# Performance work log

Measured on AMD Instinct MI355X. Metric: run time of the kernel, lower is better.

Reference implementation:

```python
import jax, jax.numpy as jnp
import numpy as np

B, T, D, H = 64, 512, 1024, 1024
FORGET_BIAS = 1.0  # tf BasicLSTMCell default


def setup_inputs() -> dict:
    key = jax.random.key(0)
    k1, k2 = jax.random.split(key)
    x = jax.random.normal(k1, (B, T, D), dtype=jnp.float32)
    W = jax.random.normal(k2, (D + H, 4 * H), dtype=jnp.float32) * 0.01  # W_stddev
    b = jnp.full((4 * H,), 0.1, dtype=jnp.float32)  # b_val
    return {"x": x, "W": W, "b": b}


def reference(x, W, b):
    # Unrolled BasicLSTMCell over num_of_cells steps, expressed as lax.scan.
    # Gate order (i, j, f, o), new_c = c*sigmoid(f+1) + sigmoid(i)*tanh(j),
    # new_h = tanh(new_c)*sigmoid(o). return_cell_out=True -> [B, T, H].
    Bx = x.shape[0]
    h0 = jnp.zeros((Bx, H), dtype=x.dtype)
    c0 = jnp.zeros((Bx, H), dtype=x.dtype)

    def step(carry, xt):  # xt: [B, D]
        c, h = carry
        z = jnp.concatenate([xt, h], axis=-1) @ W + b  # [B, 4H]
        i, j, f, o = jnp.split(z, 4, axis=-1)
        c_new = c * jax.nn.sigmoid(f + FORGET_BIAS) + jax.nn.sigmoid(i) * jnp.tanh(j)
        h_new = jnp.tanh(c_new) * jax.nn.sigmoid(o)
        return (c_new, h_new), h_new

    xs = jnp.swapaxes(x, 0, 1)  # [T, B, D]
    (_, _), hs = jax.lax.scan(step, (c0, h0), xs)  # hs: [T, B, H]
    return jnp.swapaxes(hs, 0, 1)  # [B, T, H]
```

## Files before the change

kernel.cpp:

```cpp
#include <hip/hip_runtime.h>
#include <hip/hip_bf16.h>

#define BB 64
#define TT 512
#define DD 1024
#define HH 1024

typedef __bf16 bf16x8 __attribute__((ext_vector_type(8)));
typedef float floatx4 __attribute__((ext_vector_type(4)));

__device__ __forceinline__ float sigmoidf_fast(float x) {
    return 1.0f / (1.0f + __expf(-x));
}
__device__ __forceinline__ float tanhf_fast(float x) {
    return 1.0f - 2.0f / (__expf(2.0f * x) + 1.0f);
}

__device__ __forceinline__ bool detect_f32(const void* bias) {
    return *(const unsigned*)bias == 0x3DCCCCCDu;
}

__global__ __launch_bounds__(256) void cvt_x_kernel(const void* __restrict__ xin,
                                                    const void* __restrict__ bias,
                                                    __bf16* __restrict__ xc) {
    const bool f32 = detect_f32(bias);
    size_t i = ((size_t)blockIdx.x * 256 + threadIdx.x) * 8;
    bf16x8 r;
    if (f32) {
        const float* p = (const float*)xin + i;
        float4 a = *(const float4*)p;
        float4 b = *(const float4*)(p + 4);
        r[0] = (__bf16)a.x; r[1] = (__bf16)a.y; r[2] = (__bf16)a.z; r[3] = (__bf16)a.w;
        r[4] = (__bf16)b.x; r[5] = (__bf16)b.y; r[6] = (__bf16)b.z; r[7] = (__bf16)b.w;
    } else {
        r = *(const bf16x8*)((const __bf16*)xin + i);
    }
    *(bf16x8*)(xc + i) = r;
}

#define HLOAD16(P, O0, O1, O2, O3, O4, O5, O6, O7, O8, O9, O10, O11, O12, O13, O14, O15, \
                h0, h1, h2, h3, h4, h5, h6, h7, h8, h9, h10, h11, h12, h13, h14, h15)     \
    asm volatile(                                                                         \
        "global_load_dwordx4 %0, %16, off offset:" #O0 " sc0 sc1\n\t"                     \
        "global_load_dwordx4 %1, %16, off offset:" #O1 " sc0 sc1\n\t"                     \
        "global_load_dwordx4 %2, %16, off offset:" #O2 " sc0 sc1\n\t"                     \
        "global_load_dwordx4 %3, %16, off offset:" #O3 " sc0 sc1\n\t"                     \
        "global_load_dwordx4 %4, %16, off offset:" #O4 " sc0 sc1\n\t"                     \
        "global_load_dwordx4 %5, %16, off offset:" #O5 " sc0 sc1\n\t"                     \
        "global_load_dwordx4 %6, %16, off offset:" #O6 " sc0 sc1\n\t"                     \
        "global_load_dwordx4 %7, %16, off offset:" #O7 " sc0 sc1\n\t"                     \
        "global_load_dwordx4 %8, %16, off offset:" #O8 " sc0 sc1\n\t"                     \
        "global_load_dwordx4 %9, %16, off offset:" #O9 " sc0 sc1\n\t"                     \
        "global_load_dwordx4 %10, %16, off offset:" #O10 " sc0 sc1\n\t"                   \
        "global_load_dwordx4 %11, %16, off offset:" #O11 " sc0 sc1\n\t"                   \
        "global_load_dwordx4 %12, %16, off offset:" #O12 " sc0 sc1\n\t"                   \
        "global_load_dwordx4 %13, %16, off offset:" #O13 " sc0 sc1\n\t"                   \
        "global_load_dwordx4 %14, %16, off offset:" #O14 " sc0 sc1\n\t"                   \
        "global_load_dwordx4 %15, %16, off offset:" #O15 " sc0 sc1"                       \
        : "=v"(h0), "=v"(h1), "=v"(h2), "=v"(h3), "=v"(h4), "=v"(h5), "=v"(h6), "=v"(h7), \
          "=v"(h8), "=v"(h9), "=v"(h10), "=v"(h11), "=v"(h12), "=v"(h13), "=v"(h14),      \
          "=v"(h15)                                                                       \
        : "v"(P)                                                                          \
        : "memory");                                                                      \
    asm volatile("s_waitcnt vmcnt(0)"                                                     \
        : "+v"(h0), "+v"(h1), "+v"(h2), "+v"(h3), "+v"(h4), "+v"(h5), "+v"(h6), "+v"(h7), \
          "+v"(h8), "+v"(h9), "+v"(h10), "+v"(h11), "+v"(h12), "+v"(h13), "+v"(h14),      \
          "+v"(h15));

#define HMFMA(HV, KC)                                                                 \
    acc = __builtin_amdgcn_mfma_f32_16x16x32_bf16(                                    \
        __builtin_bit_cast(bf16x8, HV),                                               \
        *(const bf16x8*)&Wlds[(((KC) + 32) * 64 + lane) * 8], acc, 0, 0, 0);

template <bool XCONV>
__global__ __launch_bounds__(256, 1)
void lstm_persistent(const void* __restrict__ x_raw,
                     const void* __restrict__ W_raw,
                     const void* __restrict__ bias_raw,
                     void* __restrict__ out_raw,
                     unsigned int* __restrict__ cnt,
                     __bf16* __restrict__ hbuf,
                     const __bf16* __restrict__ xc)
{
    const int tid  = threadIdx.x;
    const int bk   = blockIdx.x;
    const int wave = tid >> 6;
    const int lane = tid & 63;
    const int quad = lane >> 4;
    const int c    = lane & 15;
    const bool f32 = detect_f32(bias_raw);

    __shared__ __bf16 Wlds[64 * 64 * 8];
    for (int it = 0; it < 32; ++it) {
        int idx = it * 256 + tid;
        int k = idx >> 2, g = idx & 3;
        __bf16 w0, w1, w2, w3;
        if (f32) {
            float4 w4 = *(const float4*)((const float*)W_raw + k * 4096 + g * 1024 + bk * 4);
            w0 = (__bf16)w4.x; w1 = (__bf16)w4.y; w2 = (__bf16)w4.z; w3 = (__bf16)w4.w;
        } else {
            const __bf16* wp = (const __bf16*)W_raw + k * 4096 + g * 1024 + bk * 4;
            w0 = wp[0]; w1 = wp[1]; w2 = wp[2]; w3 = wp[3];
        }
        int kc = k >> 5, q = (k >> 3) & 3, j = k & 7;
        int base = (kc * 64 + q * 16 + g * 4) * 8 + j;
        Wlds[base]      = w0;
        Wlds[base + 8]  = w1;
        Wlds[base + 16] = w2;
        Wlds[base + 24] = w3;
    }
    __syncthreads();

    const int rowA  = wave * 16 + c;
    const int nOut  = bk * 4 + (c & 3);
    const int orow  = wave * 16 + (lane >> 2);
    const int ocol  = bk * 4 + (lane & 3);

    float bi, bj, bfg, bo;
    if (f32) {
        const float* bp = (const float*)bias_raw;
        bi = bp[nOut]; bj = bp[1024 + nOut]; bfg = bp[2048 + nOut] + 1.0f; bo = bp[3072 + nOut];
    } else {
        const __bf16* bp = (const __bf16*)bias_raw;
        bi = (float)bp[nOut]; bj = (float)bp[1024 + nOut];
        bfg = (float)bp[2048 + nOut] + 1.0f; bo = (float)bp[3072 + nOut];
    }

    float cst[4] = {0.f, 0.f, 0.f, 0.f};

    const __bf16* xcA = xc + (size_t)rowA * (TT * DD) + quad * 8;
    const float*  xfA = (const float*)x_raw + (size_t)rowA * (TT * DD) + quad * 8;
    float* outf = (float*)out_raw;
    __hip_bfloat16* outb = (__hip_bfloat16*)out_raw;

    for (int t = 0; t < TT; ++t) {
        floatx4 acc = {0.f, 0.f, 0.f, 0.f};

#pragma unroll 8
        for (int kc = 0; kc < 32; ++kc) {
            bf16x8 a;
            if (XCONV) {
                a = *(const bf16x8*)(xcA + (size_t)t * DD + kc * 32);
            } else {
                const float* p = xfA + (size_t)t * DD + kc * 32;
                float4 u = *(const float4*)p;
                float4 v = *(const float4*)(p + 4);
                a[0] = (__bf16)u.x; a[1] = (__bf16)u.y; a[2] = (__bf16)u.z; a[3] = (__bf16)u.w;
                a[4] = (__bf16)v.x; a[5] = (__bf16)v.y; a[6] = (__bf16)v.z; a[7] = (__bf16)v.w;
            }
            bf16x8 w = *(const bf16x8*)&Wlds[(kc * 64 + lane) * 8];
            acc = __builtin_amdgcn_mfma_f32_16x16x32_bf16(a, w, acc, 0, 0, 0);
        }

        if (t > 0) {
            if (tid == 0) {
                while (__hip_atomic_load(&cnt[t - 1], __ATOMIC_RELAXED,
                                         __HIP_MEMORY_SCOPE_AGENT) < 256u)
                    __builtin_amdgcn_s_sleep(2);
            }
            __syncthreads();
            const __bf16* hp = hbuf + (size_t)(t & 1) * (BB * HH)
                             + (size_t)rowA * HH + quad * 8;
            floatx4 h0, h1, h2, h3, h4, h5, h6, h7, h8, h9, h10, h11, h12, h13, h14, h15;
            HLOAD16(hp, 0, 64, 128, 192, 256, 320, 384, 448, 512, 576, 640, 704, 768,
                    832, 896, 960,
                    h0, h1, h2, h3, h4, h5, h6, h7, h8, h9, h10, h11, h12, h13, h14, h15)
            HMFMA(h0, 0)  HMFMA(h1, 1)  HMFMA(h2, 2)   HMFMA(h3, 3)
            HMFMA(h4, 4)  HMFMA(h5, 5)  HMFMA(h6, 6)   HMFMA(h7, 7)
            HMFMA(h8, 8)  HMFMA(h9, 9)  HMFMA(h10, 10) HMFMA(h11, 11)
            HMFMA(h12, 12) HMFMA(h13, 13) HMFMA(h14, 14) HMFMA(h15, 15)
            HLOAD16(hp, 1024, 1088, 1152, 1216, 1280, 1344, 1408, 1472, 1536, 1600,
                    1664, 1728, 1792, 1856, 1920, 1984,
                    h0, h1, h2, h3, h4, h5, h6, h7, h8, h9, h10, h11, h12, h13, h14, h15)
            HMFMA(h0, 16)  HMFMA(h1, 17)  HMFMA(h2, 18)  HMFMA(h3, 19)
            HMFMA(h4, 20)  HMFMA(h5, 21)  HMFMA(h6, 22)  HMFMA(h7, 23)
            HMFMA(h8, 24)  HMFMA(h9, 25)  HMFMA(h10, 26) HMFMA(h11, 27)
            HMFMA(h12, 28) HMFMA(h13, 29) HMFMA(h14, 30) HMFMA(h15, 31)
        }

        float hv0, hv1, hv2, hv3;
        {
#pragma unroll
            for (int r = 0; r < 4; ++r) {
                float av = acc[r];
                float jg = __shfl(av, (lane + 4) & 63, 64);
                float fg = __shfl(av, (lane + 8) & 63, 64);
                float og = __shfl(av, (lane + 12) & 63, 64);
                float I = sigmoidf_fast(av + bi);
                float J = tanhf_fast(jg + bj);
                float F = sigmoidf_fast(fg + bfg);
                float O = sigmoidf_fast(og + bo);
                float cc = cst[r] * F + I * J;
                cst[r] = cc;
                float hvr = tanhf_fast(cc) * O;
                if (r == 0) hv0 = hvr; else if (r == 1) hv1 = hvr;
                else if (r == 2) hv2 = hvr; else hv3 = hvr;
            }
        }

        int srcLane = (lane & 48) | (lane & 3);
        float t0 = __shfl(hv0, srcLane, 64);
        float t1 = __shfl(hv1, srcLane, 64);
        float t2 = __shfl(hv2, srcLane, 64);
        float t3 = __shfl(hv3, srcLane, 64);
        int rsel = (lane >> 2) & 3;
        float va = (rsel & 1) ? t1 : t0;
        float vb = (rsel & 1) ? t3 : t2;
        float hvf = (rsel & 2) ? vb : va;

        size_t oidx = (size_t)orow * (TT * HH) + (size_t)t * HH + ocol;
        if (f32) outf[oidx] = hvf;
        else     outb[oidx] = __float2bfloat16(hvf);

        {
            __bf16 hb = (__bf16)hvf;
            unsigned hbits = (unsigned)__builtin_bit_cast(unsigned short, hb);
            const __bf16* hwp = hbuf + (size_t)((t + 1) & 1) * (BB * HH)
                              + (size_t)orow * HH + ocol;
            asm volatile("global_store_short %0, %1, off sc0 sc1"
                         :: "v"(hwp), "v"(hbits) : "memory");
        }

        asm volatile("s_waitcnt vmcnt(0)" ::: "memory");
        __syncthreads();
        if (tid == 0) atomicAdd(&cnt[t], 1u);
    }
}

extern "C" void kernel_launch(void* const* d_in, const int* in_sizes, int n_in,
                              void* d_out, int out_size, void* d_ws, size_t ws_size,
                              hipStream_t stream) {
    const void* x = d_in[0];
    const void* W = d_in[1];
    const void* b = d_in[2];

    unsigned int* cnt = (unsigned int*)d_ws;
    __bf16*      hbuf = (__bf16*)((char*)d_ws + 4096);
    __bf16*      xc   = (__bf16*)((char*)d_ws + 266240);

    const size_t need = 266240 + (size_t)BB * TT * DD * 2;

    hipMemsetAsync(d_ws, 0, TT * sizeof(unsigned int), stream);
    if (ws_size >= need) {
        cvt_x_kernel<<<(BB * TT * DD / 8 + 255) / 256, 256, 0, stream>>>(x, b, xc);
        lstm_persistent<true><<<256, 256, 0, stream>>>(x, W, b, d_out, cnt, hbuf, xc);
    } else {
        lstm_persistent<false><<<256, 256, 0, stream>>>(x, W, b, d_out, cnt, hbuf, xc);
    }
}
```

Measured before the change: 5.651 ms.

## Split waves into x-projection and recurrent roles with per-wave flag sync

Halves the grid to 128 blocks of 512 threads, each owning 8 hidden columns. Four waves compute the input projection for step t while the other four wait on the previous step's h and run the recurrent MFMAs; partial sums are exchanged through LDS. The single atomic counter and block-wide barrier are replaced by per-wave flag words that are polled with vector loads. The h loads are also split into two batches with partial waits so MFMAs can start sooner. This aims to take the x-projection off the recurrent critical path and cut barrier latency, at the cost of a larger flag area that must be zeroed by memset and a block-wide barrier at every step.

Result: slower. 6.625 ms (+17.2%).

```diff
diff --git a/kernel.cpp b/kernel.cpp
--- a/kernel.cpp
+++ b/kernel.cpp
@@ -5,9 +5,12 @@
 #define TT 512
 #define DD 1024
 #define HH 1024
+#define NB 128
+#define NTHR 512
 
 typedef __bf16 bf16x8 __attribute__((ext_vector_type(8)));
 typedef float floatx4 __attribute__((ext_vector_type(4)));
+typedef unsigned int uintx4 __attribute__((ext_vector_type(4)));
 
 __device__ __forceinline__ float sigmoidf_fast(float x) {
     return 1.0f / (1.0f + __expf(-x));
@@ -38,8 +41,8 @@
     *(bf16x8*)(xc + i) = r;
 }
 
-#define HLOAD16(P, O0, O1, O2, O3, O4, O5, O6, O7, O8, O9, O10, O11, O12, O13, O14, O15, \
-                h0, h1, h2, h3, h4, h5, h6, h7, h8, h9, h10, h11, h12, h13, h14, h15)     \
+#define HISSUE16(P, O0, O1, O2, O3, O4, O5, O6, O7, O8, O9, O10, O11, O12, O13, O14, O15, \
+                 h0, h1, h2, h3, h4, h5, h6, h7, h8, h9, h10, h11, h12, h13, h14, h15)    \
     asm volatile(                                                                         \
         "global_load_dwordx4 %0, %16, off offset:" #O0 " sc0 sc1\n\t"                     \
         "global_load_dwordx4 %1, %16, off offset:" #O1 " sc0 sc1\n\t"                     \
@@ -57,53 +60,115 @@
         "global_load_dwordx4 %13, %16, off offset:" #O13 " sc0 sc1\n\t"                   \
         "global_load_dwordx4 %14, %16, off offset:" #O14 " sc0 sc1\n\t"                   \
         "global_load_dwordx4 %15, %16, off offset:" #O15 " sc0 sc1"                       \
-        : "=v"(h0), "=v"(h1), "=v"(h2), "=v"(h3), "=v"(h4), "=v"(h5), "=v"(h6), "=v"(h7), \
-          "=v"(h8), "=v"(h9), "=v"(h10), "=v"(h11), "=v"(h12), "=v"(h13), "=v"(h14),      \
-          "=v"(h15)                                                                       \
+        : "=&v"(h0), "=&v"(h1), "=&v"(h2), "=&v"(h3), "=&v"(h4), "=&v"(h5), "=&v"(h6),    \
+          "=&v"(h7), "=&v"(h8), "=&v"(h9), "=&v"(h10), "=&v"(h11), "=&v"(h12),            \
+          "=&v"(h13), "=&v"(h14), "=&v"(h15)                                              \
         : "v"(P)                                                                          \
-        : "memory");                                                                      \
-    asm volatile("s_waitcnt vmcnt(0)"                                                     \
+        : "memory");
+
+#define HWAIT16(N, h0, h1, h2, h3, h4, h5, h6, h7, h8, h9, h10, h11, h12, h13, h14, h15)  \
+    asm volatile("s_waitcnt vmcnt(" #N ")"                                                \
         : "+v"(h0), "+v"(h1), "+v"(h2), "+v"(h3), "+v"(h4), "+v"(h5), "+v"(h6), "+v"(h7), \
           "+v"(h8), "+v"(h9), "+v"(h10), "+v"(h11), "+v"(h12), "+v"(h13), "+v"(h14),      \
           "+v"(h15));
 
-#define HMFMA(HV, KC)                                                                 \
-    acc = __builtin_amdgcn_mfma_f32_16x16x32_bf16(                                    \
-        __builtin_bit_cast(bf16x8, HV),                                               \
-        *(const bf16x8*)&Wlds[(((KC) + 32) * 64 + lane) * 8], acc, 0, 0, 0);
+#define HMFMA2(HV, KCG)                                                            \
+    acc0 = __builtin_amdgcn_mfma_f32_16x16x32_bf16(                                \
+        __builtin_bit_cast(bf16x8, HV),                                            \
+        *(const bf16x8*)&Wlds[(((KCG) * 2 + 0) * 64 + lane) * 8], acc0, 0, 0, 0);  \
+    acc1 = __builtin_amdgcn_mfma_f32_16x16x32_bf16(                                \
+        __builtin_bit_cast(bf16x8, HV),                                            \
+        *(const bf16x8*)&Wlds[(((KCG) * 2 + 1) * 64 + lane) * 8], acc1, 0, 0, 0);
+
+#define GATES(ACC, BI, BJ, BFg, BO, C0, C1, C2, C3, HVF)                           \
+    {                                                                              \
+        float hv0, hv1, hv2, hv3;                                                  \
+        { float av = ACC[0];                                                       \
+          float jg = __shfl(av, (lane + 4) & 63, 64);                              \
+          float fg = __shfl(av, (lane + 8) & 63, 64);                              \
+          float og = __shfl(av, (lane + 12) & 63, 64);                             \
+          float I = sigmoidf_fast(av + BI);                                        \
+          float J = tanhf_fast(jg + BJ);                                           \
+          float F = sigmoidf_fast(fg + BFg);                                       \
+          float O = sigmoidf_fast(og + BO);                                        \
+          float cc = C0 * F + I * J; C0 = cc; hv0 = tanhf_fast(cc) * O; }          \
+        { float av = ACC[1];                                                       \
+          float jg = __shfl(av, (lane + 4) & 63, 64);                              \
+          float fg = __shfl(av, (lane + 8) & 63, 64);                              \
+          float og = __shfl(av, (lane + 12) & 63, 64);                             \
+          float I = sigmoidf_fast(av + BI);                                        \
+          float J = tanhf_fast(jg + BJ);                                           \
+          float F = sigmoidf_fast(fg + BFg);                                       \
+          float O = sigmoidf_fast(og + BO);                                        \
+          float cc = C1 * F + I * J; C1 = cc; hv1 = tanhf_fast(cc) * O; }          \
+        { float av = ACC[2];                                                       \
+          float jg = __shfl(av, (lane + 4) & 63, 64);                              \
+          float fg = __shfl(av, (lane + 8) & 63, 64);                              \
+          float og = __shfl(av, (lane + 12) & 63, 64);                             \
+          float I = sigmoidf_fast(av + BI);                                        \
+          float J = tanhf_fast(jg + BJ);                                           \
+          float F = sigmoidf_fast(fg + BFg);                                       \
+          float O = sigmoidf_fast(og + BO);                                        \
+          float cc = C2 * F + I * J; C2 = cc; hv2 = tanhf_fast(cc) * O; }          \
+        { float av = ACC[3];                                                       \
+          float jg = __shfl(av, (lane + 4) & 63, 64);                              \
+          float fg = __shfl(av, (lane + 8) & 63, 64);                              \
+          float og = __shfl(av, (lane + 12) & 63, 64);                             \
+          float I = sigmoidf_fast(av + BI);                                        \
+          float J = tanhf_fast(jg + BJ);                                           \
+          float F = sigmoidf_fast(fg + BFg);                                       \
+          float O = sigmoidf_fast(og + BO);                                        \
+          float cc = C3 * F + I * J; C3 = cc; hv3 = tanhf_fast(cc) * O; }          \
+        int srcLane = (lane & 48) | (lane & 3);                                    \
+        float t0 = __shfl(hv0, srcLane, 64);                                       \
+        float t1 = __shfl(hv1, srcLane, 64);                                       \
+        float t2 = __shfl(hv2, srcLane, 64);                                       \
+        float t3 = __shfl(hv3, srcLane, 64);                                       \
+        int rsel = (lane >> 2) & 3;                                                \
+        float va = (rsel & 1) ? t1 : t0;                                           \
+        float vb = (rsel & 1) ? t3 : t2;                                           \
+        HVF = (rsel & 2) ? vb : va;                                                \
+    }
 
 template <bool XCONV>
-__global__ __launch_bounds__(256, 1)
+__global__ __launch_bounds__(NTHR, 1)
 void lstm_persistent(const void* __restrict__ x_raw,
                      const void* __restrict__ W_raw,
                      const void* __restrict__ bias_raw,
                      void* __restrict__ out_raw,
-                     unsigned int* __restrict__ cnt,
+                     unsigned int* __restrict__ flags,
                      __bf16* __restrict__ hbuf,
                      const __bf16* __restrict__ xc)
 {
-    const int tid  = threadIdx.x;
-    const int bk   = blockIdx.x;
-    const int wave = tid >> 6;
-    const int lane = tid & 63;
-    const int quad = lane >> 4;
-    const int c    = lane & 15;
-    const bool f32 = detect_f32(bias_raw);
-
-    __shared__ __bf16 Wlds[64 * 64 * 8];
+    const int tid   = threadIdx.x;
+    const int bk    = blockIdx.x;
+    const int wave  = tid >> 6;
+    const int lane  = tid & 63;
+    const int quad  = lane >> 4;
+    const int c     = lane & 15;
+    const bool f32  = detect_f32(bias_raw);
+    const bool hrole = wave < 4;
+    const int wr    = wave & 3;
+
+    __shared__ __bf16 Wlds[64 * 2 * 512];
+    __shared__ float  xpart[2][4][2][64][4];
+
     for (int it = 0; it < 32; ++it) {
-        int idx = it * 256 + tid;
-        int k = idx >> 2, g = idx & 3;
+        int idx = it * NTHR + tid;
+        int n   = idx >> 13;
+        int r   = idx & 8191;
+        int k   = r >> 2, g = r & 3;
+        int col = g * 1024 + bk * 8 + n * 4;
         __bf16 w0, w1, w2, w3;
         if (f32) {
-            float4 w4 = *(const float4*)((const float*)W_raw + k * 4096 + g * 1024 + bk * 4);
+            float4 w4 = *(const float4*)((const float*)W_raw + (size_t)k * 4096 + col);
             w0 = (__bf16)w4.x; w1 = (__bf16)w4.y; w2 = (__bf16)w4.z; w3 = (__bf16)w4.w;
         } else {
-            const __bf16* wp = (const __bf16*)W_raw + k * 4096 + g * 1024 + bk * 4;
+            const __bf16* wp = (const __bf16*)W_raw + (size_t)k * 4096 + col;
             w0 = wp[0]; w1 = wp[1]; w2 = wp[2]; w3 = wp[3];
         }
         int kc = k >> 5, q = (k >> 3) & 3, j = k & 7;
-        int base = (kc * 64 + q * 16 + g * 4) * 8 + j;
+        int base = (((kc * 2 + n) * 64) + q * 16 + g * 4) * 8 + j;
         Wlds[base]      = w0;
         Wlds[base + 8]  = w1;
         Wlds[base + 16] = w2;
@@ -111,22 +176,29 @@
     }
     __syncthreads();
 
-    const int rowA  = wave * 16 + c;
-    const int nOut  = bk * 4 + (c & 3);
-    const int orow  = wave * 16 + (lane >> 2);
-    const int ocol  = bk * 4 + (lane & 3);
-
-    float bi, bj, bfg, bo;
-    if (f32) {
-        const float* bp = (const float*)bias_raw;
-        bi = bp[nOut]; bj = bp[1024 + nOut]; bfg = bp[2048 + nOut] + 1.0f; bo = bp[3072 + nOut];
-    } else {
-        const __bf16* bp = (const __bf16*)bias_raw;
-        bi = (float)bp[nOut]; bj = (float)bp[1024 + nOut];
-        bfg = (float)bp[2048 + nOut] + 1.0f; bo = (float)bp[3072 + nOut];
-    }
-
-    float cst[4] = {0.f, 0.f, 0.f, 0.f};
+    const int rowA = wr * 16 + c;
+    const int orow = wr * 16 + (lane >> 2);
+    const int oc0  = bk * 8 + (lane & 3);
+    const int oc1  = oc0 + 4;
+
+    float bi0, bj0, bf0, bo0, bi1, bj1, bf1, bo1;
+    float cA0 = 0.f, cA1 = 0.f, cA2 = 0.f, cA3 = 0.f;
+    float cB0 = 0.f, cB1 = 0.f, cB2 = 0.f, cB3 = 0.f;
+    if (hrole) {
+        int n0 = bk * 8 + (c & 3);
+        int n1 = n0 + 4;
+        if (f32) {
+            const float* bp = (const float*)bias_raw;
+            bi0 = bp[n0]; bj0 = bp[1024 + n0]; bf0 = bp[2048 + n0] + 1.0f; bo0 = bp[3072 + n0];
+            bi1 = bp[n1]; bj1 = bp[1024 + n1]; bf1 = bp[2048 + n1] + 1.0f; bo1 = bp[3072 + n1];
+        } else {
+            const __bf16* bp = (const __bf16*)bias_raw;
+            bi0 = (float)bp[n0]; bj0 = (float)bp[1024 + n0];
+            bf0 = (float)bp[2048 + n0] + 1.0f; bo0 = (float)bp[3072 + n0];
+            bi1 = (float)bp[n1]; bj1 = (float)bp[1024 + n1];
+            bf1 = (float)bp[2048 + n1] + 1.0f; bo1 = (float)bp[3072 + n1];
+        }
+    }
 
     const __bf16* xcA = xc + (size_t)rowA * (TT * DD) + quad * 8;
     const float*  xfA = (const float*)x_raw + (size_t)rowA * (TT * DD) + quad * 8;
@@ -134,96 +206,102 @@
     __hip_bfloat16* outb = (__hip_bfloat16*)out_raw;
 
     for (int t = 0; t < TT; ++t) {
-        floatx4 acc = {0.f, 0.f, 0.f, 0.f};
-
+        const int p = t & 1;
+        floatx4 acc0 = {0.f, 0.f, 0.f, 0.f};
+        floatx4 acc1 = {0.f, 0.f, 0.f, 0.f};
+
+        if (!hrole) {
+            floatx4 a0 = {0.f, 0.f, 0.f, 0.f};
+            floatx4 a1 = {0.f, 0.f, 0.f, 0.f};
 #pragma unroll 8
-        for (int kc = 0; kc < 32; ++kc) {
-            bf16x8 a;
-            if (XCONV) {
-                a = *(const bf16x8*)(xcA + (size_t)t * DD + kc * 32);
+            for (int kc = 0; kc < 32; ++kc) {
+                bf16x8 a;
+                if (XCONV) {
+                    a = *(const bf16x8*)(xcA + (size_t)t * DD + kc * 32);
+                } else {
+                    const float* pp = xfA + (size_t)t * DD + kc * 32;
+                    float4 u = *(const float4*)pp;
+                    float4 v = *(const float4*)(pp + 4);
+                    a[0] = (__bf16)u.x; a[1] = (__bf16)u.y; a[2] = (__bf16)u.z; a[3] = (__bf16)u.w;
+                    a[4] = (__bf16)v.x; a[5] = (__bf16)v.y; a[6] = (__bf16)v.z; a[7] = (__bf16)v.w;
+                }
+                a0 = __builtin_amdgcn_mfma_f32_16x16x32_bf16(
+                    a, *(const bf16x8*)&Wlds[((kc * 2 + 0) * 64 + lane) * 8], a0, 0, 0, 0);
+                a1 = __builtin_amdgcn_mfma_f32_16x16x32_bf16(
+                    a, *(const bf16x8*)&Wlds[((kc * 2 + 1) * 64 + lane) * 8], a1, 0, 0, 0);
+            }
+            *(floatx4*)&xpart[p][wr][0][lane][0] = a0;
+            *(floatx4*)&xpart[p][wr][1][lane][0] = a1;
+        } else if (t > 0) {
+            const unsigned int* fp = flags + (size_t)(t - 1) * 512 + (lane << 3);
+            for (;;) {
+                uintx4 fa, fb;
+                asm volatile(
+                    "global_load_dwordx4 %0, %2, off sc0 sc1\n\t"
+                    "global_load_dwordx4 %1, %2, off offset:16 sc0 sc1\n\t"
+                    "s_waitcnt vmcnt(0)"
+                    : "=&v"(fa), "=&v"(fb) : "v"(fp) : "memory");
+                unsigned ok = fa[0] & fa[1] & fa[2] & fa[3] & fb[0] & fb[1] & fb[2] & fb[3];
+                if (__all((int)ok)) break;
+                __builtin_amdgcn_s_sleep(1);
+            }
+            const __bf16* hp = hbuf + (size_t)(t & 1) * (BB * HH) + (size_t)rowA * HH + quad * 8;
+            floatx4 h0, h1, h2, h3, h4, h5, h6, h7, h8, h9, h10, h11, h12, h13, h14, h15;
+            floatx4 g0, g1, g2, g3, g4, g5, g6, g7, g8, g9, g10, g11, g12, g13, g14, g15;
+            HISSUE16(hp, 0, 64, 128, 192, 256, 320, 384, 448, 512, 576, 640, 704, 768,
+                     832, 896, 960,
+                     h0, h1, h2, h3, h4, h5, h6, h7, h8, h9, h10, h11, h12, h13, h14, h15)
+            HISSUE16(hp, 1024, 1088, 1152, 1216, 1280, 1344, 1408, 1472, 1536, 1600,
+                     1664, 1728, 1792, 1856, 1920, 1984,
+                     g0, g1, g2, g3, g4, g5, g6, g7, g8, g9, g10, g11, g12, g13, g14, g15)
+            HWAIT16(16, h0, h1, h2, h3, h4, h5, h6, h7, h8, h9, h10, h11, h12, h13, h14, h15)
+            HMFMA2(h0, 32)  HMFMA2(h1, 33)  HMFMA2(h2, 34)  HMFMA2(h3, 35)
+            HMFMA2(h4, 36)  HMFMA2(h5, 37)  HMFMA2(h6, 38)  HMFMA2(h7, 39)
+            HMFMA2(h8, 40)  HMFMA2(h9, 41)  HMFMA2(h10, 42) HMFMA2(h11, 43)
+            HMFMA2(h12, 44) HMFMA2(h13, 45) HMFMA2(h14, 46) HMFMA2(h15, 47)
+            HWAIT16(0, g0, g1, g2, g3, g4, g5, g6, g7, g8, g9, g10, g11, g12, g13, g14, g15)
+            HMFMA2(g0, 48)  HMFMA2(g1, 49)  HMFMA2(g2, 50)  HMFMA2(g3, 51)
+            HMFMA2(g4, 52)  HMFMA2(g5, 53)  HMFMA2(g6, 54)  HMFMA2(g7, 55)
+            HMFMA2(g8, 56)  HMFMA2(g9, 57)  HMFMA2(g10, 58) HMFMA2(g11, 59)
+            HMFMA2(g12, 60) HMFMA2(g13, 61) HMFMA2(g14, 62) HMFMA2(g15, 63)
+        }
+
+        __syncthreads();
+
+        if (hrole) {
+            acc0 += *(const floatx4*)&xpart[p][wr][0][lane][0];
+            acc1 += *(const floatx4*)&xpart[p][wr][1][lane][0];
+
+            float hvf0, hvf1;
+            GATES(acc0, bi0, bj0, bf0, bo0, cA0, cA1, cA2, cA3, hvf0)
+            GATES(acc1, bi1, bj1, bf1, bo1, cB0, cB1, cB2, cB3, hvf1)
+
+            {
+                __bf16 hb0 = (__bf16)hvf0, hb1 = (__bf16)hvf1;
+                unsigned b0 = (unsigned)__builtin_bit_cast(unsigned short, hb0);
+                unsigned b1 = (unsigned)__builtin_bit_cast(unsigned short, hb1);
+                const __bf16* hw = hbuf + (size_t)((t + 1) & 1) * (BB * HH) + (size_t)orow * HH;
+                asm volatile(
+                    "global_store_short %0, %2, off sc0 sc1\n\t"
+                    "global_store_short %1, %3, off sc0 sc1"
+                    :: "v"(hw + oc0), "v"(hw + oc1), "v"(b0), "v"(b1) : "memory");
+            }
+            asm volatile("s_waitcnt vmcnt(0)" ::: "memory");
+            if (lane == 0) {
+                unsigned one = 1u;
+                const unsigned int* fw = flags + (size_t)t * 512 + (bk * 4 + wr);
+                asm volatile("global_store_dword %0, %1, off sc0 sc1"
+                             :: "v"(fw), "v"(one) : "memory");
+            }
+            size_t ob = (size_t)orow * (TT * HH) + (size_t)t * HH;
+            if (f32) {
+                outf[ob + oc0] = hvf0;
+                outf[ob + oc1] = hvf1;
             } else {
-                const float* p = xfA + (size_t)t * DD + kc * 32;
-                float4 u = *(const float4*)p;
-                float4 v = *(const float4*)(p + 4);
-                a[0] = (__bf16)u.x; a[1] = (__bf16)u.y; a[2] = (__bf16)u.z; a[3] = (__bf16)u.w;
-                a[4] = (__bf16)v.x; a[5] = (__bf16)v.y; a[6] = (__bf16)v.z; a[7] = (__bf16)v.w;
-            }
-            bf16x8 w = *(const bf16x8*)&Wlds[(kc * 64 + lane) * 8];
-            acc = __builtin_amdgcn_mfma_f32_16x16x32_bf16(a, w, acc, 0, 0, 0);
+                outb[ob + oc0] = __float2bfloat16(hvf0);
+                outb[ob + oc1] = __float2bfloat16(hvf1);
+            }
         }
-
-        if (t > 0) {
-            if (tid == 0) {
-                while (__hip_atomic_load(&cnt[t - 1], __ATOMIC_RELAXED,
-                                         __HIP_MEMORY_SCOPE_AGENT) < 256u)
-                    __builtin_amdgcn_s_sleep(2);
-            }
-            __syncthreads();
-            const __bf16* hp = hbuf + (size_t)(t & 1) * (BB * HH)
-                             + (size_t)rowA * HH + quad * 8;
-            floatx4 h0, h1, h2, h3, h4, h5, h6, h7, h8, h9, h10, h11, h12, h13, h14, h15;
-            HLOAD16(hp, 0, 64, 128, 192, 256, 320, 384, 448, 512, 576, 640, 704, 768,
-                    832, 896, 960,
-                    h0, h1, h2, h3, h4, h5, h6, h7, h8, h9, h10, h11, h12, h13, h14, h15)
-            HMFMA(h0, 0)  HMFMA(h1, 1)  HMFMA(h2, 2)   HMFMA(h3, 3)
-            HMFMA(h4, 4)  HMFMA(h5, 5)  HMFMA(h6, 6)   HMFMA(h7, 7)
-            HMFMA(h8, 8)  HMFMA(h9, 9)  HMFMA(h10, 10) HMFMA(h11, 11)
-            HMFMA(h12, 12) HMFMA(h13, 13) HMFMA(h14, 14) HMFMA(h15, 15)
-            HLOAD16(hp, 1024, 1088, 1152, 1216, 1280, 1344, 1408, 1472, 1536, 1600,
-                    1664, 1728, 1792, 1856, 1920, 1984,
-                    h0, h1, h2, h3, h4, h5, h6, h7, h8, h9, h10, h11, h12, h13, h14, h15)
-            HMFMA(h0, 16)  HMFMA(h1, 17)  HMFMA(h2, 18)  HMFMA(h3, 19)
-            HMFMA(h4, 20)  HMFMA(h5, 21)  HMFMA(h6, 22)  HMFMA(h7, 23)
-            HMFMA(h8, 24)  HMFMA(h9, 25)  HMFMA(h10, 26) HMFMA(h11, 27)
-            HMFMA(h12, 28) HMFMA(h13, 29) HMFMA(h14, 30) HMFMA(h15, 31)
-        }
-
-        float hv0, hv1, hv2, hv3;
-        {
-#pragma unroll
-            for (int r = 0; r < 4; ++r) {
-                float av = acc[r];
-                float jg = __shfl(av, (lane + 4) & 63, 64);
-                float fg = __shfl(av, (lane + 8) & 63, 64);
-                float og = __shfl(av, (lane + 12) & 63, 64);
-                float I = sigmoidf_fast(av + bi);
-                float J = tanhf_fast(jg + bj);
-                float F = sigmoidf_fast(fg + bfg);
-                float O = sigmoidf_fast(og + bo);
-                float cc = cst[r] * F + I * J;
-                cst[r] = cc;
-                float hvr = tanhf_fast(cc) * O;
-                if (r == 0) hv0 = hvr; else if (r == 1) hv1 = hvr;
-                else if (r == 2) hv2 = hvr; else hv3 = hvr;
-            }
-        }
-
-        int srcLane = (lane & 48) | (lane & 3);
-        float t0 = __shfl(hv0, srcLane, 64);
-        float t1 = __shfl(hv1, srcLane, 64);
-        float t2 = __shfl(hv2, srcLane, 64);
-        float t3 = __shfl(hv3, srcLane, 64);
-        int rsel = (lane >> 2) & 3;
-        float va = (rsel & 1) ? t1 : t0;
-        float vb = (rsel & 1) ? t3 : t2;
-        float hvf = (rsel & 2) ? vb : va;
-
-        size_t oidx = (size_t)orow * (TT * HH) + (size_t)t * HH + ocol;
-        if (f32) outf[oidx] = hvf;
-        else     outb[oidx] = __float2bfloat16(hvf);
-
-        {
-            __bf16 hb = (__bf16)hvf;
-            unsigned hbits = (unsigned)__builtin_bit_cast(unsigned short, hb);
-            const __bf16* hwp = hbuf + (size_t)((t + 1) & 1) * (BB * HH)
-                              + (size_t)orow * HH + ocol;
-            asm volatile("global_store_short %0, %1, off sc0 sc1"
-                         :: "v"(hwp), "v"(hbits) : "memory");
-        }
-
-        asm volatile("s_waitcnt vmcnt(0)" ::: "memory");
-        __syncthreads();
-        if (tid == 0) atomicAdd(&cnt[t], 1u);
     }
 }
 
@@ -234,17 +312,17 @@
     const void* W = d_in[1];
     const void* b = d_in[2];
 
-    unsigned int* cnt = (unsigned int*)d_ws;
-    __bf16*      hbuf = (__bf16*)((char*)d_ws + 4096);
-    __bf16*      xc   = (__bf16*)((char*)d_ws + 266240);
-
-    const size_t need = 266240 + (size_t)BB * TT * DD * 2;
-
-    hipMemsetAsync(d_ws, 0, TT * sizeof(unsigned int), stream);
+    unsigned int* flags = (unsigned int*)d_ws;
+    __bf16*      hbuf   = (__bf16*)((char*)d_ws + 1048576);
+    __bf16*      xc     = (__bf16*)((char*)d_ws + 1310720);
+
+    const size_t need = 1310720 + (size_t)BB * TT * DD * 2;
+
+    hipMemsetAsync(d_ws, 0, 1048576, stream);
     if (ws_size >= need) {
         cvt_x_kernel<<<(BB * TT * DD / 8 + 255) / 256, 256, 0, stream>>>(x, b, xc);
-        lstm_persistent<true><<<256, 256, 0, stream>>>(x, W, b, d_out, cnt, hbuf, xc);
+        lstm_persistent<true><<<NB, NTHR, 0, stream>>>(x, W, b, d_out, flags, hbuf, xc);
     } else {
-        lstm_persistent<false><<<256, 256, 0, stream>>>(x, W, b, d_out, cnt, hbuf, xc);
-    }
-}
+        lstm_persistent<false><<<NB, NTHR, 0, stream>>>(x, W, b, d_out, flags, hbuf, xc);
+    }
+}
```

## Split grid barrier into padded group counters and pipeline h loads with dual accumulators

Applied to the files above, without the earlier changes.

The single per-step atomic counter becomes 16 group counters padded onto separate cache lines, one per 16 blocks. Wave 0 polls all 16 in parallel with a wave-wide vote, which cuts contention on a single hot address. All 32 h loads are issued up front with a partial vmcnt wait, so the second half's latency overlaps the first half's MFMAs. Accumulation is split across two accumulators to shorten the MFMA dependency chain. The cost is a larger workspace and memset, plus more live registers.

Result: slower. 5.813 ms (+2.9%).

```diff
diff --git a/kernel.cpp b/kernel.cpp
--- a/kernel.cpp
+++ b/kernel.cpp
@@ -5,6 +5,8 @@
 #define TT 512
 #define DD 1024
 #define HH 1024
+#define NG 16
+#define GSTRIDE 32
 
 typedef __bf16 bf16x8 __attribute__((ext_vector_type(8)));
 typedef float floatx4 __attribute__((ext_vector_type(4)));
@@ -38,8 +40,8 @@
     *(bf16x8*)(xc + i) = r;
 }
 
-#define HLOAD16(P, O0, O1, O2, O3, O4, O5, O6, O7, O8, O9, O10, O11, O12, O13, O14, O15, \
-                h0, h1, h2, h3, h4, h5, h6, h7, h8, h9, h10, h11, h12, h13, h14, h15)     \
+#define HISSUE16(P, O0, O1, O2, O3, O4, O5, O6, O7, O8, O9, O10, O11, O12, O13, O14, O15, \
+                 h0, h1, h2, h3, h4, h5, h6, h7, h8, h9, h10, h11, h12, h13, h14, h15)    \
     asm volatile(                                                                         \
         "global_load_dwordx4 %0, %16, off offset:" #O0 " sc0 sc1\n\t"                     \
         "global_load_dwordx4 %1, %16, off offset:" #O1 " sc0 sc1\n\t"                     \
@@ -57,20 +59,22 @@
         "global_load_dwordx4 %13, %16, off offset:" #O13 " sc0 sc1\n\t"                   \
         "global_load_dwordx4 %14, %16, off offset:" #O14 " sc0 sc1\n\t"                   \
         "global_load_dwordx4 %15, %16, off offset:" #O15 " sc0 sc1"                       \
-        : "=v"(h0), "=v"(h1), "=v"(h2), "=v"(h3), "=v"(h4), "=v"(h5), "=v"(h6), "=v"(h7), \
-          "=v"(h8), "=v"(h9), "=v"(h10), "=v"(h11), "=v"(h12), "=v"(h13), "=v"(h14),      \
-          "=v"(h15)                                                                       \
+        : "=&v"(h0), "=&v"(h1), "=&v"(h2), "=&v"(h3), "=&v"(h4), "=&v"(h5), "=&v"(h6),    \
+          "=&v"(h7), "=&v"(h8), "=&v"(h9), "=&v"(h10), "=&v"(h11), "=&v"(h12),            \
+          "=&v"(h13), "=&v"(h14), "=&v"(h15)                                              \
         : "v"(P)                                                                          \
-        : "memory");                                                                      \
-    asm volatile("s_waitcnt vmcnt(0)"                                                     \
+        : "memory");
+
+#define HWAIT16(N, h0, h1, h2, h3, h4, h5, h6, h7, h8, h9, h10, h11, h12, h13, h14, h15)  \
+    asm volatile("s_waitcnt vmcnt(" #N ")"                                                \
         : "+v"(h0), "+v"(h1), "+v"(h2), "+v"(h3), "+v"(h4), "+v"(h5), "+v"(h6), "+v"(h7), \
           "+v"(h8), "+v"(h9), "+v"(h10), "+v"(h11), "+v"(h12), "+v"(h13), "+v"(h14),      \
           "+v"(h15));
 
-#define HMFMA(HV, KC)                                                                 \
-    acc = __builtin_amdgcn_mfma_f32_16x16x32_bf16(                                    \
-        __builtin_bit_cast(bf16x8, HV),                                               \
-        *(const bf16x8*)&Wlds[(((KC) + 32) * 64 + lane) * 8], acc, 0, 0, 0);
+#define HMFMA(ACC, HV, KC)                                                          \
+    ACC = __builtin_amdgcn_mfma_f32_16x16x32_bf16(                                  \
+        __builtin_bit_cast(bf16x8, HV),                                             \
+        *(const bf16x8*)&Wlds[(((KC) + 32) * 64 + lane) * 8], ACC, 0, 0, 0);
 
 template <bool XCONV>
 __global__ __launch_bounds__(256, 1)
@@ -78,7 +82,7 @@
                      const void* __restrict__ W_raw,
                      const void* __restrict__ bias_raw,
                      void* __restrict__ out_raw,
-                     unsigned int* __restrict__ cnt,
+                     unsigned int* __restrict__ gcnt,
                      __bf16* __restrict__ hbuf,
                      const __bf16* __restrict__ xc)
 {
@@ -134,7 +138,8 @@
     __hip_bfloat16* outb = (__hip_bfloat16*)out_raw;
 
     for (int t = 0; t < TT; ++t) {
-        floatx4 acc = {0.f, 0.f, 0.f, 0.f};
+        floatx4 accA = {0.f, 0.f, 0.f, 0.f};
+        floatx4 accB = {0.f, 0.f, 0.f, 0.f};
 
 #pragma unroll 8
         for (int kc = 0; kc < 32; ++kc) {
@@ -149,34 +154,49 @@
                 a[4] = (__bf16)v.x; a[5] = (__bf16)v.y; a[6] = (__bf16)v.z; a[7] = (__bf16)v.w;
             }
             bf16x8 w = *(const bf16x8*)&Wlds[(kc * 64 + lane) * 8];
-            acc = __builtin_amdgcn_mfma_f32_16x16x32_bf16(a, w, acc, 0, 0, 0);
+            if (kc & 1)
+                accB = __builtin_amdgcn_mfma_f32_16x16x32_bf16(a, w, accB, 0, 0, 0);
+            else
+                accA = __builtin_amdgcn_mfma_f32_16x16x32_bf16(a, w, accA, 0, 0, 0);
         }
 
         if (t > 0) {
-            if (tid == 0) {
-                while (__hip_atomic_load(&cnt[t - 1], __ATOMIC_RELAXED,
-                                         __HIP_MEMORY_SCOPE_AGENT) < 256u)
-                    __builtin_amdgcn_s_sleep(2);
+            if (wave == 0) {
+                const unsigned int* gp =
+                    gcnt + (size_t)(t - 1) * (NG * GSTRIDE) + (size_t)(lane & 15) * GSTRIDE;
+                for (;;) {
+                    unsigned v = NG;
+                    if (lane < NG)
+                        v = __hip_atomic_load(gp, __ATOMIC_RELAXED, __HIP_MEMORY_SCOPE_AGENT);
+                    if (__all((int)(v >= NG))) break;
+                    __builtin_amdgcn_s_sleep(1);
+                }
             }
             __syncthreads();
+
             const __bf16* hp = hbuf + (size_t)(t & 1) * (BB * HH)
                              + (size_t)rowA * HH + quad * 8;
             floatx4 h0, h1, h2, h3, h4, h5, h6, h7, h8, h9, h10, h11, h12, h13, h14, h15;
-            HLOAD16(hp, 0, 64, 128, 192, 256, 320, 384, 448, 512, 576, 640, 704, 768,
-                    832, 896, 960,
-                    h0, h1, h2, h3, h4, h5, h6, h7, h8, h9, h10, h11, h12, h13, h14, h15)
-            HMFMA(h0, 0)  HMFMA(h1, 1)  HMFMA(h2, 2)   HMFMA(h3, 3)
-            HMFMA(h4, 4)  HMFMA(h5, 5)  HMFMA(h6, 6)   HMFMA(h7, 7)
-            HMFMA(h8, 8)  HMFMA(h9, 9)  HMFMA(h10, 10) HMFMA(h11, 11)
-            HMFMA(h12, 12) HMFMA(h13, 13) HMFMA(h14, 14) HMFMA(h15, 15)
-            HLOAD16(hp, 1024, 1088, 1152, 1216, 1280, 1344, 1408, 1472, 1536, 1600,
-                    1664, 1728, 1792, 1856, 1920, 1984,
-                    h0, h1, h2, h3, h4, h5, h6, h7, h8, h9, h10, h11, h12, h13, h14, h15)
-            HMFMA(h0, 16)  HMFMA(h1, 17)  HMFMA(h2, 18)  HMFMA(h3, 19)
-            HMFMA(h4, 20)  HMFMA(h5, 21)  HMFMA(h6, 22)  HMFMA(h7, 23)
-            HMFMA(h8, 24)  HMFMA(h9, 25)  HMFMA(h10, 26) HMFMA(h11, 27)
-            HMFMA(h12, 28) HMFMA(h13, 29) HMFMA(h14, 30) HMFMA(h15, 31)
-        }
+            floatx4 g0, g1, g2, g3, g4, g5, g6, g7, g8, g9, g10, g11, g12, g13, g14, g15;
+            HISSUE16(hp, 0, 64, 128, 192, 256, 320, 384, 448, 512, 576, 640, 704, 768,
+                     832, 896, 960,
+                     h0, h1, h2, h3, h4, h5, h6, h7, h8, h9, h10, h11, h12, h13, h14, h15)
+            HISSUE16(hp, 1024, 1088, 1152, 1216, 1280, 1344, 1408, 1472, 1536, 1600,
+                     1664, 1728, 1792, 1856, 1920, 1984,
+                     g0, g1, g2, g3, g4, g5, g6, g7, g8, g9, g10, g11, g12, g13, g14, g15)
+            HWAIT16(16, h0, h1, h2, h3, h4, h5, h6, h7, h8, h9, h10, h11, h12, h13, h14, h15)
+            HMFMA(accA, h0, 0)   HMFMA(accB, h1, 1)   HMFMA(accA, h2, 2)   HMFMA(accB, h3, 3)
+            HMFMA(accA, h4, 4)   HMFMA(accB, h5, 5)   HMFMA(accA, h6, 6)   HMFMA(accB, h7, 7)
+            HMFMA(accA, h8, 8)   HMFMA(accB, h9, 9)   HMFMA(accA, h10, 10) HMFMA(accB, h11, 11)
+            HMFMA(accA, h12, 12) HMFMA(accB, h13, 13) HMFMA(accA, h14, 14) HMFMA(accB, h15, 15)
+            HWAIT16(0, g0, g1, g2, g3, g4, g5, g6, g7, g8, g9, g10, g11, g12, g13, g14, g15)
+            HMFMA(accA, g0, 16)  HMFMA(accB, g1, 17)  HMFMA(accA, g2, 18)  HMFMA(accB, g3, 19)
+            HMFMA(accA, g4, 20)  HMFMA(accB, g5, 21)  HMFMA(accA, g6, 22)  HMFMA(accB, g7, 23)
+            HMFMA(accA, g8, 24)  HMFMA(accB, g9, 25)  HMFMA(accA, g10, 26) HMFMA(accB, g11, 27)
+            HMFMA(accA, g12, 28) HMFMA(accB, g13, 29) HMFMA(accA, g14, 30) HMFMA(accB, g15, 31)
+        }
+
+        floatx4 acc = accA + accB;
 
         float hv0, hv1, hv2, hv3;
         {
@@ -223,7 +243,8 @@
 
         asm volatile("s_waitcnt vmcnt(0)" ::: "memory");
         __syncthreads();
-        if (tid == 0) atomicAdd(&cnt[t], 1u);
+        if (tid == 0)
+            atomicAdd(&gcnt[(size_t)t * (NG * GSTRIDE) + (size_t)(bk >> 4) * GSTRIDE], 1u);
     }
 }
 
@@ -234,17 +255,17 @@
     const void* W = d_in[1];
     const void* b = d_in[2];
 
-    unsigned int* cnt = (unsigned int*)d_ws;
-    __bf16*      hbuf = (__bf16*)((char*)d_ws + 4096);
-    __bf16*      xc   = (__bf16*)((char*)d_ws + 266240);
-
-    const size_t need = 266240 + (size_t)BB * TT * DD * 2;
-
-    hipMemsetAsync(d_ws, 0, TT * sizeof(unsigned int), stream);
+    unsigned int* gcnt = (unsigned int*)d_ws;
+    __bf16*      hbuf  = (__bf16*)((char*)d_ws + 1048576);
+    __bf16*      xc    = (__bf16*)((char*)d_ws + 1310720);
+
+    const size_t need = 1310720 + (size_t)BB * TT * DD * 2;
+
+    hipMemsetAsync(d_ws, 0, (size_t)TT * NG * GSTRIDE * 4, stream);
     if (ws_size >= need) {
         cvt_x_kernel<<<(BB * TT * DD / 8 + 255) / 256, 256, 0, stream>>>(x, b, xc);
-        lstm_persistent<true><<<256, 256, 0, stream>>>(x, W, b, d_out, cnt, hbuf, xc);
+        lstm_persistent<true><<<256, 256, 0, stream>>>(x, W, b, d_out, gcnt, hbuf, xc);
     } else {
-        lstm_persistent<false><<<256, 256, 0, stream>>>(x, W, b, d_out, cnt, hbuf, xc);
-    }
-}
+        lstm_persistent<false><<<256, 256, 0, stream>>>(x, W, b, d_out, gcnt, hbuf, xc);
+    }
+}
```
